# Performance work log

Measured on AMD Instinct MI355X. Metric: run time of the kernel, lower is better.

Reference implementation:

```python
import jax, jax.numpy as jnp
import numpy as np

N_NODES = 50000
NUM_FEATURE = 256
NUM_HIDDEN = 128
NUM_CLASSES = 16
N_EDGES = 1600000


def gcn_conv(x, W, b, src, dst, deg_inv_sqrt, n_nodes):
    # GCNConv: h = x @ W ; out[i] = sum_{j->i} norm_ji * h[j] + b
    # with symmetric normalization over the self-loop-augmented graph.
    h = x @ W  # [N, out_ch]
    norm = deg_inv_sqrt[src] * deg_inv_sqrt[dst]  # [E']
    msgs = h[src] * norm[:, None]  # [E', out_ch] (dominant intermediate)
    out = jax.ops.segment_sum(msgs, dst, num_segments=n_nodes)
    return out + b


def setup_inputs() -> dict:
    key = jax.random.key(0)
    k_x, k_e, k_w1, k_b1, k_w2, k_b2 = jax.random.split(key, 6)
    x = jax.random.normal(k_x, (N_NODES, NUM_FEATURE), dtype=jnp.float32)
    edge_index = jax.random.randint(k_e, (2, N_EDGES), 0, N_NODES, dtype=jnp.int64)
    # Glorot init like PyG's GCNConv linear
    s1 = (6.0 / (NUM_FEATURE + NUM_HIDDEN)) ** 0.5
    s2 = (6.0 / (NUM_HIDDEN + NUM_CLASSES)) ** 0.5
    W1 = jax.random.uniform(k_w1, (NUM_FEATURE, NUM_HIDDEN), jnp.float32, -s1, s1)
    b1 = jnp.zeros((NUM_HIDDEN,), jnp.float32)
    W2 = jax.random.uniform(k_w2, (NUM_HIDDEN, NUM_CLASSES), jnp.float32, -s2, s2)
    b2 = jnp.zeros((NUM_CLASSES,), jnp.float32)
    return {"x": x, "edge_index": edge_index, "W1": W1, "b1": b1, "W2": W2, "b2": b2}


def reference(x, edge_index, W1, b1, W2, b2):
    n = x.shape[0]
    # add self-loops (done inside GCNConv for each layer; identical both times)
    loops = jnp.arange(n, dtype=edge_index.dtype)
    src = jnp.concatenate([edge_index[0], loops])
    dst = jnp.concatenate([edge_index[1], loops])
    deg = jax.ops.segment_sum(jnp.ones_like(dst, dtype=x.dtype), dst, num_segments=n)
    deg_inv_sqrt = jnp.where(deg > 0, jax.lax.rsqrt(deg), 0.0)

    h = jax.nn.relu(gcn_conv(x, W1, b1, src, dst, deg_inv_sqrt, n))
    # F.dropout with training=False is the identity (eval-mode baseline)
    logits = gcn_conv(h, W2, b2, src, dst, deg_inv_sqrt, n)
    return jax.nn.log_softmax(logits, axis=1)
```

## Files before the change

kernel.cpp:

```cpp
#include <hip/hip_runtime.h>
#include <hip/hip_fp16.h>
#include <math.h>

#define NF 256
#define NH 128
#define NC 16
#define NB 391
#define NBLK 512

typedef __attribute__((ext_vector_type(8))) short bf16x8;
typedef __attribute__((ext_vector_type(4))) float f32x4;
typedef __attribute__((ext_vector_type(2))) float f32v2;

__device__ __forceinline__ unsigned f2b(float f) {
    unsigned u = __float_as_uint(f);
    return (u + 0x7FFFu + ((u >> 16) & 1u)) >> 16;
}
__device__ __forceinline__ unsigned packt(float a, float b) {
    return (__float_as_uint(a) >> 16) | (__float_as_uint(b) & 0xFFFF0000u);
}
union h2u { __half2 h; unsigned u; };
__device__ __forceinline__ __half2 uh(unsigned u) { h2u c; c.u = u; return c.h; }
__device__ __forceinline__ unsigned hu(__half2 h) { h2u c; c.h = h; return c.u; }

__global__ void prep_kernel(const int* __restrict__ dst, int* __restrict__ hist, int E,
                            const float* __restrict__ W1, unsigned short* __restrict__ W1T,
                            unsigned* __restrict__ h1c32, unsigned* __restrict__ h2sb,
                            int* __restrict__ ubase, int N) {
    __shared__ int h[NB];
    int b = blockIdx.x, tid = threadIdx.x;
    if (b < NBLK) {
        for (int i = tid; i < NB; i += 256) h[i] = 0;
        __syncthreads();
        int e0 = (int)((long long)b * E / NBLK), e1 = (int)((long long)(b + 1) * E / NBLK);
        for (int e = e0 + tid; e < e1; e += 256)
            atomicAdd(&h[dst[e] >> 7], 1);
        __syncthreads();
        for (int i = tid; i < NB; i += 256) hist[b * NB + i] = h[i];
    } else {
        int idx = (b - NBLK) * 256 + tid;
        int n = idx >> 8, k = idx & 255;
        W1T[n * 256 + k] = (unsigned short)f2b(W1[(size_t)k * NH + n]);
        if (idx < 32) {
            int q = idx >> 4, j = idx & 15;
            h1c32[(size_t)q * (N + 1) * 16 + (size_t)N * 16 + j] = 0u;
        } else if (idx < 40) {
            h2sb[(size_t)N * 8 + (idx - 32)] = 0u;
        } else if (idx == 40) {
            ubase[NB] = E;
        }
    }
}

__global__ void scanR_kernel(const int* __restrict__ hist, int* __restrict__ bsum) {
    __shared__ int sm[NBLK];
    int k = blockIdx.x, t = threadIdx.x;
    sm[t] = hist[t * NB + k];
    __syncthreads();
    for (int off = NBLK / 2; off > 0; off >>= 1) {
        if (t < off) sm[t] += sm[t + off];
        __syncthreads();
    }
    if (t == 0) bsum[k] = sm[0];
}

__global__ void scanCB_kernel(const int* __restrict__ bsum, int* __restrict__ hist,
                              int* __restrict__ ubase, int* __restrict__ pbase) {
    __shared__ int sr[NBLK];
    __shared__ int sp[NBLK];
    __shared__ int ubs;
    int k = blockIdx.x, t = threadIdx.x;
    int vu = (t < k) ? bsum[t] : 0;
    int vp = (t < k) ? (((vu + 7) & ~7) + 904) : 0;
    sr[t] = vu; sp[t] = vp;
    __syncthreads();
    for (int off = NBLK / 2; off > 0; off >>= 1) {
        if (t < off) { sr[t] += sr[t + off]; sp[t] += sp[t + off]; }
        __syncthreads();
    }
    if (t == 0) { ubs = sr[0]; ubase[k] = sr[0]; pbase[k] = sp[0]; }
    __syncthreads();
    int ub = ubs;
    int v = hist[t * NB + k];
    sr[t] = v;
    __syncthreads();
    for (int off = 1; off < NBLK; off <<= 1) {
        int u = (t >= off) ? sr[t - off] : 0;
        __syncthreads();
        sr[t] += u;
        __syncthreads();
    }
    hist[t * NB + k] = ub + sr[t] - v;
}

__global__ void passB_kernel(const int* __restrict__ src, const int* __restrict__ dst,
                             const int* __restrict__ hist, unsigned* __restrict__ ebuf,
                             int E) {
    __shared__ int cur[NB];
    int b = blockIdx.x;
    for (int i = threadIdx.x; i < NB; i += 256) cur[i] = hist[b * NB + i];
    __syncthreads();
    int e0 = (int)((long long)b * E / NBLK), e1 = (int)((long long)(b + 1) * E / NBLK);
    for (int e = e0 + (int)threadIdx.x; e < e1; e += 256) {
        int d = dst[e];
        int pos = atomicAdd(&cur[d >> 7], 1);
        ebuf[pos] = ((unsigned)d << 16) | (unsigned)src[e];
    }
}

__global__ void passC_kernel(const unsigned* __restrict__ ebuf, const int* __restrict__ ubase,
                             const int* __restrict__ pbase, int* __restrict__ rowptr,
                             int* __restrict__ degs, float* __restrict__ dis,
                             unsigned short* __restrict__ colidx, int N) {
    __shared__ int h[128];
    __shared__ int s2[128];
    __shared__ int curp[128];
    int k = blockIdx.x, t = threadIdx.x;
    if (t < 128) h[t] = 0;
    __syncthreads();
    int e0 = ubase[k], e1 = ubase[k + 1];
    for (int e = e0 + t; e < e1; e += 256)
        atomicAdd(&h[(ebuf[e] >> 16) & 127], 1);
    __syncthreads();
    int v = (t < 128) ? h[t] : 0;
    int pd = (v + 7) & ~7;
    if (t < 128) s2[t] = pd;
    __syncthreads();
    for (int off = 1; off < 128; off <<= 1) {
        int u = (t < 128 && t >= off) ? s2[t - off] : 0;
        __syncthreads();
        if (t < 128) s2[t] += u;
        __syncthreads();
    }
    if (t < 128) {
        int start = pbase[k] + s2[t] - pd;
        int node = k * 128 + t;
        if (node < N) {
            rowptr[node] = start;
            degs[node] = v;
            dis[node] = rsqrtf((float)(v + 1));
        }
        curp[t] = start;
    }
    __syncthreads();
    for (int e = e0 + t; e < e1; e += 256) {
        unsigned w = ebuf[e];
        int dl = (w >> 16) & 127;
        int pos = atomicAdd(&curp[dl], 1);
        colidx[pos] = (unsigned short)(w & 0xFFFFu);
    }
    __syncthreads();
    if (t < 128) {
        int endp = pbase[k] + s2[t];
        for (int q = curp[t]; q < endp; ++q) colidx[q] = (unsigned short)N;
    }
}

__global__ __launch_bounds__(256) void gemm1_mfma_kernel(
    const float* __restrict__ x, const unsigned short* __restrict__ W1T,
    const float* __restrict__ dis, unsigned char* __restrict__ h1c, int N) {
    __shared__ char sx[32768];
    int tid = threadIdx.x;
    int wid = tid >> 6, lane = tid & 63;

    for (int it = 0; it < 8; ++it) {
        int lr = it * 4 + wid;
        int grow = blockIdx.x * 32 + lr;
        if (grow >= N) grow = N - 1;
        int fsw = (lr & 7) << 1;
        const char* gp = (const char*)x + (size_t)grow * 1024 + ((lane ^ fsw) << 4);
        __builtin_amdgcn_global_load_lds(gp, sx + lr * 1024 + lane * 16, 16, 0, 0);
    }
    __syncthreads();

    int lrow = lane & 15, lk = lane >> 4;
    int rt = wid & 1, nh = wid >> 1;
    int lr = rt * 16 + lrow;
    int fr = (lr & 7) << 1;
    const float4* lds4 = (const float4*)sx;

    bf16x8 a[8];
#pragma unroll
    for (int kk = 0; kk < 8; ++kk) {
        int v = (kk * 8 + lk * 2) ^ fr;
        float4 lo = lds4[lr * 64 + v];
        float4 hi = lds4[lr * 64 + v + 1];
        union { unsigned u[4]; bf16x8 vv; } av;
        av.u[0] = packt(lo.x, lo.y);
        av.u[1] = packt(lo.z, lo.w);
        av.u[2] = packt(hi.x, hi.y);
        av.u[3] = packt(hi.z, hi.w);
        a[kk] = av.vv;
    }

    f32x4 acc[4];
#pragma unroll
    for (int t = 0; t < 4; ++t) acc[t] = (f32x4){0.f, 0.f, 0.f, 0.f};

#pragma unroll
    for (int nt = 0; nt < 4; ++nt) {
        int n = nh * 64 + nt * 16 + lrow;
        const unsigned short* wp = W1T + (size_t)n * 256 + lk * 8;
        bf16x8 b0 = *(const bf16x8*)(wp + 0 * 32);
        bf16x8 b1 = *(const bf16x8*)(wp + 1 * 32);
        bf16x8 b2 = *(const bf16x8*)(wp + 2 * 32);
        bf16x8 b3 = *(const bf16x8*)(wp + 3 * 32);
        bf16x8 b4 = *(const bf16x8*)(wp + 4 * 32);
        bf16x8 b5 = *(const bf16x8*)(wp + 5 * 32);
        bf16x8 b6 = *(const bf16x8*)(wp + 6 * 32);
        bf16x8 b7 = *(const bf16x8*)(wp + 7 * 32);
        acc[nt] = __builtin_amdgcn_mfma_f32_16x16x32_bf16(a[0], b0, acc[nt], 0, 0, 0);
        acc[nt] = __builtin_amdgcn_mfma_f32_16x16x32_bf16(a[1], b1, acc[nt], 0, 0, 0);
        acc[nt] = __builtin_amdgcn_mfma_f32_16x16x32_bf16(a[2], b2, acc[nt], 0, 0, 0);
        acc[nt] = __builtin_amdgcn_mfma_f32_16x16x32_bf16(a[3], b3, acc[nt], 0, 0, 0);
        acc[nt] = __builtin_amdgcn_mfma_f32_16x16x32_bf16(a[4], b4, acc[nt], 0, 0, 0);
        acc[nt] = __builtin_amdgcn_mfma_f32_16x16x32_bf16(a[5], b5, acc[nt], 0, 0, 0);
        acc[nt] = __builtin_amdgcn_mfma_f32_16x16x32_bf16(a[6], b6, acc[nt], 0, 0, 0);
        acc[nt] = __builtin_amdgcn_mfma_f32_16x16x32_bf16(a[7], b7, acc[nt], 0, 0, 0);
    }

    int rb = blockIdx.x * 32;
    int crow0 = rb + rt * 16 + lk * 4;
#pragma unroll
    for (int r = 0; r < 4; ++r) {
        int row = crow0 + r;
        if (row < N) {
            float dr = dis[row];
            size_t base = ((size_t)nh * (N + 1) + row) * 64;
#pragma unroll
            for (int nt = 0; nt < 4; ++nt) {
                float v = acc[nt][r] * dr;
                int pk = __builtin_amdgcn_cvt_pk_fp8_f32(v, v, 0, 0);
                h1c[base + nt * 16 + lrow] = (unsigned char)(pk & 0xFF);
            }
        }
    }
}

__global__ __launch_bounds__(256) void aggall_kernel(
    const int* __restrict__ rowptr, const int* __restrict__ degs,
    const unsigned short* __restrict__ colidx,
    const unsigned char* __restrict__ h1c, __half2* __restrict__ aggT, int N, int bps) {
    int p = blockIdx.x / bps;
    int i = (blockIdx.x - p * bps) * 16 + (threadIdx.x >> 4);
    if (i >= N) return;
    int l = threadIdx.x & 15;
    const unsigned* slab = (const unsigned*)(h1c + (size_t)p * (N + 1) * 64);
    unsigned sv = slab[(size_t)i * 16 + l];
    f32v2 c0 = __builtin_amdgcn_cvt_pk_f32_fp8((int)sv, 0);
    f32v2 c1 = __builtin_amdgcn_cvt_pk_f32_fp8((int)sv, 1);
    float f0 = c0.x, f1 = c0.y, f2 = c1.x, f3 = c1.y;
    int e = rowptr[i];
    int cnt8 = (degs[i] + 7) >> 3;
    if (cnt8 > 0) {
        uint4 w = *reinterpret_cast<const uint4*>(colidx + e);
        for (int b = 1; b < cnt8; ++b) {
            uint4 wn = *reinterpret_cast<const uint4*>(colidx + e + 8 * b);
            int a0 = w.x & 0xFFFF, a1 = w.x >> 16, a2 = w.y & 0xFFFF, a3 = w.y >> 16;
            int a4 = w.z & 0xFFFF, a5 = w.z >> 16, a6 = w.w & 0xFFFF, a7 = w.w >> 16;
            unsigned g0 = slab[(size_t)a0 * 16 + l];
            unsigned g1 = slab[(size_t)a1 * 16 + l];
            unsigned g2 = slab[(size_t)a2 * 16 + l];
            unsigned g3 = slab[(size_t)a3 * 16 + l];
            unsigned g4 = slab[(size_t)a4 * 16 + l];
            unsigned g5 = slab[(size_t)a5 * 16 + l];
            unsigned g6 = slab[(size_t)a6 * 16 + l];
            unsigned g7 = slab[(size_t)a7 * 16 + l];
            f32v2 d;
            d = __builtin_amdgcn_cvt_pk_f32_fp8((int)g0, 0); f0 += d.x; f1 += d.y;
            d = __builtin_amdgcn_cvt_pk_f32_fp8((int)g0, 1); f2 += d.x; f3 += d.y;
            d = __builtin_amdgcn_cvt_pk_f32_fp8((int)g1, 0); f0 += d.x; f1 += d.y;
            d = __builtin_amdgcn_cvt_pk_f32_fp8((int)g1, 1); f2 += d.x; f3 += d.y;
            d = __builtin_amdgcn_cvt_pk_f32_fp8((int)g2, 0); f0 += d.x; f1 += d.y;
            d = __builtin_amdgcn_cvt_pk_f32_fp8((int)g2, 1); f2 += d.x; f3 += d.y;
            d = __builtin_amdgcn_cvt_pk_f32_fp8((int)g3, 0); f0 += d.x; f1 += d.y;
            d = __builtin_amdgcn_cvt_pk_f32_fp8((int)g3, 1); f2 += d.x; f3 += d.y;
            d = __builtin_amdgcn_cvt_pk_f32_fp8((int)g4, 0); f0 += d.x; f1 += d.y;
            d = __builtin_amdgcn_cvt_pk_f32_fp8((int)g4, 1); f2 += d.x; f3 += d.y;
            d = __builtin_amdgcn_cvt_pk_f32_fp8((int)g5, 0); f0 += d.x; f1 += d.y;
            d = __builtin_amdgcn_cvt_pk_f32_fp8((int)g5, 1); f2 += d.x; f3 += d.y;
            d = __builtin_amdgcn_cvt_pk_f32_fp8((int)g6, 0); f0 += d.x; f1 += d.y;
            d = __builtin_amdgcn_cvt_pk_f32_fp8((int)g6, 1); f2 += d.x; f3 += d.y;
            d = __builtin_amdgcn_cvt_pk_f32_fp8((int)g7, 0); f0 += d.x; f1 += d.y;
            d = __builtin_amdgcn_cvt_pk_f32_fp8((int)g7, 1); f2 += d.x; f3 += d.y;
            w = wn;
        }
        {
            int a0 = w.x & 0xFFFF, a1 = w.x >> 16, a2 = w.y & 0xFFFF, a3 = w.y >> 16;
            int a4 = w.z & 0xFFFF, a5 = w.z >> 16, a6 = w.w & 0xFFFF, a7 = w.w >> 16;
            unsigned g0 = slab[(size_t)a0 * 16 + l];
            unsigned g1 = slab[(size_t)a1 * 16 + l];
            unsigned g2 = slab[(size_t)a2 * 16 + l];
            unsigned g3 = slab[(size_t)a3 * 16 + l];
            unsigned g4 = slab[(size_t)a4 * 16 + l];
            unsigned g5 = slab[(size_t)a5 * 16 + l];
            unsigned g6 = slab[(size_t)a6 * 16 + l];
            unsigned g7 = slab[(size_t)a7 * 16 + l];
            f32v2 d;
            d = __builtin_amdgcn_cvt_pk_f32_fp8((int)g0, 0); f0 += d.x; f1 += d.y;
            d = __builtin_amdgcn_cvt_pk_f32_fp8((int)g0, 1); f2 += d.x; f3 += d.y;
            d = __builtin_amdgcn_cvt_pk_f32_fp8((int)g1, 0); f0 += d.x; f1 += d.y;
            d = __builtin_amdgcn_cvt_pk_f32_fp8((int)g1, 1); f2 += d.x; f3 += d.y;
            d = __builtin_amdgcn_cvt_pk_f32_fp8((int)g2, 0); f0 += d.x; f1 += d.y;
            d = __builtin_amdgcn_cvt_pk_f32_fp8((int)g2, 1); f2 += d.x; f3 += d.y;
            d = __builtin_amdgcn_cvt_pk_f32_fp8((int)g3, 0); f0 += d.x; f1 += d.y;
            d = __builtin_amdgcn_cvt_pk_f32_fp8((int)g3, 1); f2 += d.x; f3 += d.y;
            d = __builtin_amdgcn_cvt_pk_f32_fp8((int)g4, 0); f0 += d.x; f1 += d.y;
            d = __builtin_amdgcn_cvt_pk_f32_fp8((int)g4, 1); f2 += d.x; f3 += d.y;
            d = __builtin_amdgcn_cvt_pk_f32_fp8((int)g5, 0); f0 += d.x; f1 += d.y;
            d = __builtin_amdgcn_cvt_pk_f32_fp8((int)g5, 1); f2 += d.x; f3 += d.y;
            d = __builtin_amdgcn_cvt_pk_f32_fp8((int)g6, 0); f0 += d.x; f1 += d.y;
            d = __builtin_amdgcn_cvt_pk_f32_fp8((int)g6, 1); f2 += d.x; f3 += d.y;
            d = __builtin_amdgcn_cvt_pk_f32_fp8((int)g7, 0); f0 += d.x; f1 += d.y;
            d = __builtin_amdgcn_cvt_pk_f32_fp8((int)g7, 1); f2 += d.x; f3 += d.y;
        }
    }
    __half2 h01 = __floats2half2_rn(f0, f1);
    __half2 h23 = __floats2half2_rn(f2, f3);
    size_t base = ((size_t)(p * 2 + (l >> 3)) * N + i) * 16 + ((2 * l) & 15);
    *reinterpret_cast<uint2*>(aggT + base) = make_uint2(hu(h01), hu(h23));
}

__global__ __launch_bounds__(256) void relu_gemm2_kernel(
    const __half2* __restrict__ aggT, const float* __restrict__ dis,
    const float* __restrict__ b1, const float* __restrict__ W2,
    __half2* __restrict__ h2sb, int N) {
    __shared__ float sW2[NH * NC];
    __shared__ float srow[4][NH];
    int tid = threadIdx.x;
    for (int k = tid; k < NH * NC; k += 256) sW2[k] = W2[k];
    __syncthreads();

    int wid = tid >> 6, lane = tid & 63;
    int i = blockIdx.x * 4 + wid;
    if (i >= N) return;
    int p = lane >> 4, l16 = lane & 15;
    float2 f = __half22float2(aggT[((size_t)p * N + i) * 16 + l16]);
    float di = dis[i];
    int c0 = p * 32 + l16 * 2;
    srow[wid][c0]     = fmaxf(di * f.x + b1[c0], 0.f);
    srow[wid][c0 + 1] = fmaxf(di * f.y + b1[c0 + 1], 0.f);
    int j = lane & 15, q = lane >> 4;
    const float* rw = srow[wid];
    float pacc = 0.f;
#pragma unroll
    for (int cc = 0; cc < 32; ++cc) {
        int c = q * 32 + cc;
        pacc += rw[c] * sW2[c * NC + j];
    }
    pacc += __shfl_xor(pacc, 16, 64);
    pacc += __shfl_xor(pacc, 32, 64);
    float dp = di * pacc;
    float plo = __shfl(dp, (lane << 1) & 63, 64);
    float phi = __shfl(dp, ((lane << 1) | 1) & 63, 64);
    if (lane < 8) h2sb[(size_t)i * 8 + lane] = __floats2half2_rn(plo, phi);
}

__global__ void layer2_kernel(const int* __restrict__ rowptr, const int* __restrict__ degs,
                              const unsigned short* __restrict__ colidx,
                              const uint2* __restrict__ h2sb2, const float* __restrict__ dis,
                              const float* __restrict__ b2, float* __restrict__ out, int N) {
    int t = blockIdx.x * 256 + threadIdx.x;
    int i = t >> 2;
    if (i >= N) return;
    int j4 = t & 3;
    int e = rowptr[i];
    int cnt4 = (degs[i] + 3) >> 2;
    uint2 sv = h2sb2[(size_t)i * 4 + j4];
    __half2 acc0 = uh(sv.x), acc1 = uh(sv.y);
    if (cnt4 > 0) {
        uint2 w = *reinterpret_cast<const uint2*>(colidx + e);
        for (int b = 1; b < cnt4; ++b) {
            uint2 wn = *reinterpret_cast<const uint2*>(colidx + e + 4 * b);
            int a0 = w.x & 0xFFFF, a1 = w.x >> 16;
            int a2 = w.y & 0xFFFF, a3 = w.y >> 16;
            uint2 g0 = h2sb2[(size_t)a0 * 4 + j4];
            uint2 g1 = h2sb2[(size_t)a1 * 4 + j4];
            uint2 g2 = h2sb2[(size_t)a2 * 4 + j4];
            uint2 g3 = h2sb2[(size_t)a3 * 4 + j4];
            acc0 = __hadd2(acc0, __hadd2(__hadd2(uh(g0.x), uh(g1.x)),
                                         __hadd2(uh(g2.x), uh(g3.x))));
            acc1 = __hadd2(acc1, __hadd2(__hadd2(uh(g0.y), uh(g1.y)),
                                         __hadd2(uh(g2.y), uh(g3.y))));
            w = wn;
        }
        int a0 = w.x & 0xFFFF, a1 = w.x >> 16;
        int a2 = w.y & 0xFFFF, a3 = w.y >> 16;
        uint2 g0 = h2sb2[(size_t)a0 * 4 + j4];
        uint2 g1 = h2sb2[(size_t)a1 * 4 + j4];
        uint2 g2 = h2sb2[(size_t)a2 * 4 + j4];
        uint2 g3 = h2sb2[(size_t)a3 * 4 + j4];
        acc0 = __hadd2(acc0, __hadd2(__hadd2(uh(g0.x), uh(g1.x)),
                                     __hadd2(uh(g2.x), uh(g3.x))));
        acc1 = __hadd2(acc1, __hadd2(__hadd2(uh(g0.y), uh(g1.y)),
                                     __hadd2(uh(g2.y), uh(g3.y))));
    }
    float2 f0 = __half22float2(acc0);
    float2 f1 = __half22float2(acc1);
    float di = dis[i];
    float4 bb = *reinterpret_cast<const float4*>(b2 + 4 * j4);
    float l0 = di * f0.x + bb.x;
    float l1 = di * f0.y + bb.y;
    float l2 = di * f1.x + bb.z;
    float l3 = di * f1.y + bb.w;
    float m = fmaxf(fmaxf(l0, l1), fmaxf(l2, l3));
    m = fmaxf(m, __shfl_xor(m, 1, 64));
    m = fmaxf(m, __shfl_xor(m, 2, 64));
    float s = __expf(l0 - m) + __expf(l1 - m) + __expf(l2 - m) + __expf(l3 - m);
    s += __shfl_xor(s, 1, 64);
    s += __shfl_xor(s, 2, 64);
    float lse = m + __logf(s);
    float4 o = make_float4(l0 - lse, l1 - lse, l2 - lse, l3 - lse);
    *reinterpret_cast<float4*>(out + (size_t)i * NC + 4 * j4) = o;
}

extern "C" void kernel_launch(void* const* d_in, const int* in_sizes, int n_in,
                              void* d_out, int out_size, void* d_ws, size_t ws_size,
                              hipStream_t stream) {
    const float* x  = (const float*)d_in[0];
    const int*   ei = (const int*)d_in[1];
    const float* W1 = (const float*)d_in[2];
    const float* b1 = (const float*)d_in[3];
    const float* W2 = (const float*)d_in[4];
    const float* b2 = (const float*)d_in[5];
    float* out = (float*)d_out;

    const int N = in_sizes[0] / NF;
    const int E = in_sizes[1] / 2;
    const int* src = ei;
    const int* dst = ei + E;

    unsigned char*  h1c    = (unsigned char*)d_ws;
    __half2*        aggT   = (__half2*)(h1c + (size_t)2 * (N + 1) * 64);
    __half2*        h2sb   = aggT + (size_t)4 * N * 16;
    float*          dis    = (float*)(h2sb + (size_t)(N + 1) * 8);
    int*            degs   = (int*)(dis + N);
    int*            rowptr = degs + N;
    int*            hist   = rowptr + N;
    int*            bsum   = hist + NBLK * NB;
    int*            ubase  = bsum + NB;
    int*            pbase  = ubase + NB + 1;
    unsigned*       ebuf   = (unsigned*)(pbase + NB + 2);
    unsigned short* colidx = (unsigned short*)(ebuf + E);
    unsigned short* W1T    = colidx + (size_t)E + 360000;

    prep_kernel<<<NBLK + 128, 256, 0, stream>>>(dst, hist, E, W1, W1T,
                                                (unsigned*)h1c, (unsigned*)h2sb,
                                                ubase, N);
    scanR_kernel<<<NB, NBLK, 0, stream>>>(hist, bsum);
    scanCB_kernel<<<NB, NBLK, 0, stream>>>(bsum, hist, ubase, pbase);
    passB_kernel<<<NBLK, 256, 0, stream>>>(src, dst, hist, ebuf, E);
    passC_kernel<<<NB, 256, 0, stream>>>(ebuf, ubase, pbase, rowptr, degs, dis, colidx, N);

    gemm1_mfma_kernel<<<(N + 31) / 32, 256, 0, stream>>>(x, W1T, dis, h1c, N);

    const int bps = (N + 15) / 16;
    aggall_kernel<<<2 * bps, 256, 0, stream>>>(rowptr, degs, colidx, h1c, aggT, N, bps);

    relu_gemm2_kernel<<<(N + 3) / 4, 256, 0, stream>>>(aggT, dis, b1, W2, h2sb, N);

    layer2_kernel<<<((size_t)N * 4 + 255) / 256, 256, 0, stream>>>(rowptr, degs, colidx,
                                                                   (const uint2*)h2sb, dis, b2, out, N);
}
```

Baseline: 142.4 us.

## Make gemm1 persistent with double-buffered LDS prefetch of x tiles

```diff
diff --git a/kernel.cpp b/kernel.cpp
--- a/kernel.cpp
+++ b/kernel.cpp
@@ -158,82 +158,109 @@
 
 __global__ __launch_bounds__(256) void gemm1_mfma_kernel(
     const float* __restrict__ x, const unsigned short* __restrict__ W1T,
-    const float* __restrict__ dis, unsigned char* __restrict__ h1c, int N) {
-    __shared__ char sx[32768];
+    const float* __restrict__ dis, unsigned char* __restrict__ h1c, int N, int NT) {
+    __shared__ char sx[65536];
     int tid = threadIdx.x;
     int wid = tid >> 6, lane = tid & 63;
-
-    for (int it = 0; it < 8; ++it) {
-        int lr = it * 4 + wid;
-        int grow = blockIdx.x * 32 + lr;
-        if (grow >= N) grow = N - 1;
-        int fsw = (lr & 7) << 1;
-        const char* gp = (const char*)x + (size_t)grow * 1024 + ((lane ^ fsw) << 4);
-        __builtin_amdgcn_global_load_lds(gp, sx + lr * 1024 + lane * 16, 16, 0, 0);
-    }
-    __syncthreads();
+    int G = gridDim.x;
 
     int lrow = lane & 15, lk = lane >> 4;
     int rt = wid & 1, nh = wid >> 1;
     int lr = rt * 16 + lrow;
     int fr = (lr & 7) << 1;
-    const float4* lds4 = (const float4*)sx;
-
-    bf16x8 a[8];
-#pragma unroll
-    for (int kk = 0; kk < 8; ++kk) {
-        int v = (kk * 8 + lk * 2) ^ fr;
-        float4 lo = lds4[lr * 64 + v];
-        float4 hi = lds4[lr * 64 + v + 1];
-        union { unsigned u[4]; bf16x8 vv; } av;
-        av.u[0] = packt(lo.x, lo.y);
-        av.u[1] = packt(lo.z, lo.w);
-        av.u[2] = packt(hi.x, hi.y);
-        av.u[3] = packt(hi.z, hi.w);
-        a[kk] = av.vv;
-    }
-
-    f32x4 acc[4];
-#pragma unroll
-    for (int t = 0; t < 4; ++t) acc[t] = (f32x4){0.f, 0.f, 0.f, 0.f};
-
-#pragma unroll
-    for (int nt = 0; nt < 4; ++nt) {
-        int n = nh * 64 + nt * 16 + lrow;
-        const unsigned short* wp = W1T + (size_t)n * 256 + lk * 8;
-        bf16x8 b0 = *(const bf16x8*)(wp + 0 * 32);
-        bf16x8 b1 = *(const bf16x8*)(wp + 1 * 32);
-        bf16x8 b2 = *(const bf16x8*)(wp + 2 * 32);
-        bf16x8 b3 = *(const bf16x8*)(wp + 3 * 32);
-        bf16x8 b4 = *(const bf16x8*)(wp + 4 * 32);
-        bf16x8 b5 = *(const bf16x8*)(wp + 5 * 32);
-        bf16x8 b6 = *(const bf16x8*)(wp + 6 * 32);
-        bf16x8 b7 = *(const bf16x8*)(wp + 7 * 32);
-        acc[nt] = __builtin_amdgcn_mfma_f32_16x16x32_bf16(a[0], b0, acc[nt], 0, 0, 0);
-        acc[nt] = __builtin_amdgcn_mfma_f32_16x16x32_bf16(a[1], b1, acc[nt], 0, 0, 0);
-        acc[nt] = __builtin_amdgcn_mfma_f32_16x16x32_bf16(a[2], b2, acc[nt], 0, 0, 0);
-        acc[nt] = __builtin_amdgcn_mfma_f32_16x16x32_bf16(a[3], b3, acc[nt], 0, 0, 0);
-        acc[nt] = __builtin_amdgcn_mfma_f32_16x16x32_bf16(a[4], b4, acc[nt], 0, 0, 0);
-        acc[nt] = __builtin_amdgcn_mfma_f32_16x16x32_bf16(a[5], b5, acc[nt], 0, 0, 0);
-        acc[nt] = __builtin_amdgcn_mfma_f32_16x16x32_bf16(a[6], b6, acc[nt], 0, 0, 0);
-        acc[nt] = __builtin_amdgcn_mfma_f32_16x16x32_bf16(a[7], b7, acc[nt], 0, 0, 0);
-    }
-
-    int rb = blockIdx.x * 32;
-    int crow0 = rb + rt * 16 + lk * 4;
-#pragma unroll
-    for (int r = 0; r < 4; ++r) {
-        int row = crow0 + r;
-        if (row < N) {
-            float dr = dis[row];
-            size_t base = ((size_t)nh * (N + 1) + row) * 64;
-#pragma unroll
-            for (int nt = 0; nt < 4; ++nt) {
-                float v = acc[nt][r] * dr;
-                int pk = __builtin_amdgcn_cvt_pk_fp8_f32(v, v, 0, 0);
-                h1c[base + nt * 16 + lrow] = (unsigned char)(pk & 0xFF);
+
+    int t0 = blockIdx.x;
+    if (t0 < NT) {
+        for (int it = 0; it < 8; ++it) {
+            int r = it * 4 + wid;
+            int grow = t0 * 32 + r;
+            if (grow >= N) grow = N - 1;
+            int fsw = (r & 7) << 1;
+            const char* gp = (const char*)x + (size_t)grow * 1024 + ((lane ^ fsw) << 4);
+            __builtin_amdgcn_global_load_lds(gp, sx + r * 1024 + lane * 16, 16, 0, 0);
+        }
+    }
+
+    int cur = 0;
+    for (int t = t0; t < NT; t += G) {
+        int tn = t + G;
+        char* nxtbuf = sx + (cur ^ 1) * 32768;
+        if (tn < NT) {
+            for (int it = 0; it < 8; ++it) {
+                int r = it * 4 + wid;
+                int grow = tn * 32 + r;
+                if (grow >= N) grow = N - 1;
+                int fsw = (r & 7) << 1;
+                const char* gp = (const char*)x + (size_t)grow * 1024 + ((lane ^ fsw) << 4);
+                __builtin_amdgcn_global_load_lds(gp, nxtbuf + r * 1024 + lane * 16, 16, 0, 0);
             }
-        }
+            asm volatile("s_waitcnt vmcnt(8)" ::: "memory");
+        } else {
+            asm volatile("s_waitcnt vmcnt(0)" ::: "memory");
+        }
+        __builtin_amdgcn_sched_barrier(0);
+        __builtin_amdgcn_s_barrier();
+
+        const float4* lds4 = (const float4*)(sx + cur * 32768);
+        bf16x8 a[8];
+#pragma unroll
+        for (int kk = 0; kk < 8; ++kk) {
+            int v = (kk * 8 + lk * 2) ^ fr;
+            float4 lo = lds4[lr * 64 + v];
+            float4 hi = lds4[lr * 64 + v + 1];
+            union { unsigned u[4]; bf16x8 vv; } av;
+            av.u[0] = packt(lo.x, lo.y);
+            av.u[1] = packt(lo.z, lo.w);
+            av.u[2] = packt(hi.x, hi.y);
+            av.u[3] = packt(hi.z, hi.w);
+            a[kk] = av.vv;
+        }
+
+        f32x4 acc[4];
+#pragma unroll
+        for (int q = 0; q < 4; ++q) acc[q] = (f32x4){0.f, 0.f, 0.f, 0.f};
+
+#pragma unroll
+        for (int nt = 0; nt < 4; ++nt) {
+            int n = nh * 64 + nt * 16 + lrow;
+            const unsigned short* wp = W1T + (size_t)n * 256 + lk * 8;
+            bf16x8 b0 = *(const bf16x8*)(wp + 0 * 32);
+            bf16x8 b1 = *(const bf16x8*)(wp + 1 * 32);
+            bf16x8 b2 = *(const bf16x8*)(wp + 2 * 32);
+            bf16x8 b3 = *(const bf16x8*)(wp + 3 * 32);
+            bf16x8 b4 = *(const bf16x8*)(wp + 4 * 32);
+            bf16x8 b5 = *(const bf16x8*)(wp + 5 * 32);
+            bf16x8 b6 = *(const bf16x8*)(wp + 6 * 32);
+            bf16x8 b7 = *(const bf16x8*)(wp + 7 * 32);
+            acc[nt] = __builtin_amdgcn_mfma_f32_16x16x32_bf16(a[0], b0, acc[nt], 0, 0, 0);
+            acc[nt] = __builtin_amdgcn_mfma_f32_16x16x32_bf16(a[1], b1, acc[nt], 0, 0, 0);
+            acc[nt] = __builtin_amdgcn_mfma_f32_16x16x32_bf16(a[2], b2, acc[nt], 0, 0, 0);
+            acc[nt] = __builtin_amdgcn_mfma_f32_16x16x32_bf16(a[3], b3, acc[nt], 0, 0, 0);
+            acc[nt] = __builtin_amdgcn_mfma_f32_16x16x32_bf16(a[4], b4, acc[nt], 0, 0, 0);
+            acc[nt] = __builtin_amdgcn_mfma_f32_16x16x32_bf16(a[5], b5, acc[nt], 0, 0, 0);
+            acc[nt] = __builtin_amdgcn_mfma_f32_16x16x32_bf16(a[6], b6, acc[nt], 0, 0, 0);
+            acc[nt] = __builtin_amdgcn_mfma_f32_16x16x32_bf16(a[7], b7, acc[nt], 0, 0, 0);
+        }
+
+        int rb = t * 32;
+        int crow0 = rb + rt * 16 + lk * 4;
+#pragma unroll
+        for (int r = 0; r < 4; ++r) {
+            int row = crow0 + r;
+            if (row < N) {
+                float dr = dis[row];
+                size_t base = ((size_t)nh * (N + 1) + row) * 64;
+#pragma unroll
+                for (int nt = 0; nt < 4; ++nt) {
+                    float v = acc[nt][r] * dr;
+                    int pk = __builtin_amdgcn_cvt_pk_fp8_f32(v, v, 0, 0);
+                    h1c[base + nt * 16 + lrow] = (unsigned char)(pk & 0xFF);
+                }
+            }
+        }
+        __builtin_amdgcn_sched_barrier(0);
+        __builtin_amdgcn_s_barrier();
+        cur ^= 1;
     }
 }
 
@@ -452,7 +479,8 @@
     passB_kernel<<<NBLK, 256, 0, stream>>>(src, dst, hist, ebuf, E);
     passC_kernel<<<NB, 256, 0, stream>>>(ebuf, ubase, pbase, rowptr, degs, dis, colidx, N);
 
-    gemm1_mfma_kernel<<<(N + 31) / 32, 256, 0, stream>>>(x, W1T, dis, h1c, N);
+    const int NT = (N + 31) / 32;
+    gemm1_mfma_kernel<<<512, 256, 0, stream>>>(x, W1T, dis, h1c, N, NT);
 
     const int bps = (N + 15) / 16;
     aggall_kernel<<<2 * bps, 256, 0, stream>>>(rowptr, degs, colidx, h1c, aggT, N, bps);
```

Result: no change. 143.0 us (+0.4%).
